# Kernel optimization log

Hardware: AMD Instinct MI355X
Metric: run time of the kernel (lower is better)

## Reference

```python
import jax, jax.numpy as jnp
import numpy as np
from jax import lax

N, D, NUM_SPEC, NUM_HOPS = 8192, 256, 32, 3
ETA, EPS, LN_EPS = 0.5, 0.5, 1e-5


def setup_inputs() -> dict:
    key = jax.random.key(0)
    ks = jax.random.split(key, 4)
    H = jax.random.normal(ks[0], (N, D), dtype=jnp.float32)
    # normalized adjacency proxy: scale so spectral norm is O(1) and hops stay stable
    A = jax.random.normal(ks[1], (N, N), dtype=jnp.float32) / jnp.sqrt(jnp.float32(N))
    # orthonormal-ish eigenvector columns
    V = jax.random.normal(ks[2], (N, NUM_SPEC), dtype=jnp.float32)
    V = V / jnp.linalg.norm(V, axis=0, keepdims=True)
    eigvals = jax.random.uniform(ks[3], (NUM_SPEC,), dtype=jnp.float32, maxval=2.0)
    return {
        "H": H,
        "A": A,
        "V": V,
        "eigvals": eigvals,
        "spec_logits": jnp.zeros((NUM_SPEC,), jnp.float32),
        "lap_logits": jnp.full((NUM_SPEC,), 0.1, jnp.float32),
        "hop_weights": jnp.full((NUM_HOPS + 1,), 1.0 / (NUM_HOPS + 1), jnp.float32),
        "threshold": jnp.full((D,), 0.05, jnp.float32),
        "ln_gamma": jnp.ones((D,), jnp.float32),
        "ln_beta": jnp.zeros((D,), jnp.float32),
    }


def reference(H, A, V, eigvals, spec_logits, lap_logits, hop_weights, threshold, ln_gamma, ln_beta):
    n, d = H.shape
    num_hops = hop_weights.shape[0] - 1

    # hop propagation: hops[k] = A^k H, shape [K, n, d] with K = num_hops+1
    def step(Hc, _):
        Hn = A @ Hc
        return Hn, Hn
    _, rest = lax.scan(step, H, None, length=num_hops)
    hops = jnp.concatenate([H[None], rest], axis=0)  # [K, n, d]

    hop_w = jax.nn.softmax(hop_weights)          # [K]
    spec_w = jax.nn.softmax(spec_logits)         # [S]
    lap_lams = jax.nn.softplus(lap_logits)       # [S]
    coeff = jnp.float32(d) / (jnp.float32(n) * jnp.float32(EPS) ** 2)

    # Phi[k,s,:] = v_s^T H_k  -> batched rank-1 projections
    Phi = jnp.einsum('ns,knd->ksd', V, hops)     # [K, S, d]

    # M = I + coeff * phi phi^T, batched small [d,d] SPD solves
    eye = jnp.eye(d, dtype=H.dtype)
    M = eye + coeff * jnp.einsum('ksi,ksj->ksij', Phi, Phi)  # [K,S,d,d]
    # phi @ M^{-1} == M^{-1} phi (M symmetric)
    q = coeff * jnp.linalg.solve(M, Phi[..., None])[..., 0]  # [K,S,d]

    # grad_R_total = sum_{k,s} hop_w[k] spec_w[s] v_s q_{k,s}^T = V @ T_R
    T_R = spec_w[:, None] * jnp.einsum('k,ksd->sd', hop_w, q)       # [S,d]
    grad_R = V @ T_R                                                 # [n,d]

    # grad_L_total = sum_{k,s} hop_w[k] lap_lams[s] eig_s v_s phi_{k,s}^T
    T_L = (lap_lams * eigvals)[:, None] * jnp.einsum('k,ksd->sd', hop_w, Phi)
    grad_L = V @ T_L

    H_half = H + ETA * grad_R - ETA * grad_L

    # soft threshold (proximal L1)
    thr = threshold[None, :]
    H_out = jnp.sign(H_half) * jax.nn.relu(jnp.abs(H_half) - thr)

    # LayerNorm over last dim
    mu = jnp.mean(H_out, axis=-1, keepdims=True)
    var = jnp.var(H_out, axis=-1, keepdims=True)
    H_out = (H_out - mu) / jnp.sqrt(var + LN_EPS) * ln_gamma + ln_beta
    return (H_out, lax.stop_gradient(hop_w), lax.stop_gradient(spec_w))
```

## Files before the change

kernel.cpp:

```cpp
#include <hip/hip_runtime.h>
#include <hip/hip_bf16.h>
#include <stdint.h>

#define NN 8192
#define DIM 256
#define NSPEC 32
#define ETA 0.5f
#define COEFF 0.125f
#define LNEPS 1e-5f

typedef __attribute__((ext_vector_type(8))) short bf16x8;
typedef __attribute__((ext_vector_type(4))) float f32x4;

__device__ __forceinline__ unsigned short bf2u(__hip_bfloat16 b) {
    union { __hip_bfloat16 b; unsigned short u; } c; c.b = b; return c.u;
}
__device__ __forceinline__ __hip_bfloat16 u2bf(unsigned short u) {
    union { __hip_bfloat16 b; unsigned short u; } c; c.u = u; return c.b;
}

__device__ __forceinline__ void async16(const void* g, void* l) {
    __builtin_amdgcn_global_load_lds(
        (const __attribute__((address_space(1))) void*)g,
        (__attribute__((address_space(3))) void*)l, 16, 0, 0);
}

__global__ void castT_A(const float* __restrict__ A, __hip_bfloat16* __restrict__ AT) {
    __shared__ unsigned short tile[64 * 66];
    int r0 = blockIdx.x * 64, c0 = blockIdx.y * 64;
    int t = threadIdx.x;
    for (int i = 0; i < 16; ++i) {
        int idx = i * 256 + t;
        int r = idx >> 6, c = idx & 63;
        tile[r * 66 + c] = bf2u(__float2bfloat16(A[(long)(r0 + r) * NN + c0 + c]));
    }
    __syncthreads();
    for (int i = 0; i < 16; ++i) {
        int idx = i * 256 + t;
        int c = idx >> 6, r = idx & 63;
        AT[(long)(c0 + c) * NN + r0 + r] = u2bf(tile[r * 66 + c]);
    }
}

__global__ void trans_V(const float* __restrict__ V, __hip_bfloat16* __restrict__ VT) {
    __shared__ float tile[64 * 33];
    int n0 = blockIdx.x * 64;
    int t = threadIdx.x;
    for (int i = 0; i < 8; ++i) {
        int idx = i * 256 + t;
        tile[(idx >> 5) * 33 + (idx & 31)] = V[(long)(n0 + (idx >> 5)) * NSPEC + (idx & 31)];
    }
    __syncthreads();
    for (int i = 0; i < 8; ++i) {
        int idx = i * 256 + t;
        int s = idx >> 6, r = idx & 63;
        VT[(long)s * NN + n0 + r] = __float2bfloat16(tile[r * 33 + s]);
    }
}

#define BM 128
#define BKH 128
#define HSPLIT 8
#define HKC (NN / HSPLIT)
#define HITERS (HKC / BKH)

__launch_bounds__(256, 2)
__global__ void gemm_hopW(const __hip_bfloat16* __restrict__ AT,
                          const __hip_bfloat16* __restrict__ WT,
                          float* __restrict__ P) {
    __shared__ __align__(16) __hip_bfloat16 As[2][BM * BKH];
    __shared__ __align__(16) __hip_bfloat16 Ws[2][NSPEC * BKH];
    const int t = threadIdx.x;
    const int w = t >> 6, l = t & 63;
    const int wm = w & 1, wn = w >> 1;
    const long gm0 = (long)blockIdx.x * BM;
    const long kbase = (long)blockIdx.y * HKC;

    const int lr4 = l >> 4;
    const int lg = l & 15;

    auto stage = [&](int buf, long kpos) {
#pragma unroll
        for (int c = 0; c < 8; ++c) {
            int rb = w * 32 + c * 4;
            int row = rb + lr4;
            async16(AT + (gm0 + row) * (long)NN + kpos + ((lg ^ (row & 15)) << 3),
                    &As[buf][rb * BKH]);
        }
#pragma unroll
        for (int c = 0; c < 2; ++c) {
            int rb = w * 8 + c * 4;
            int row = rb + lr4;
            async16(WT + (long)row * NN + kpos + ((lg ^ (row & 15)) << 3),
                    &Ws[buf][rb * BKH]);
        }
    };

    f32x4 acc[4];
#pragma unroll
    for (int mt = 0; mt < 4; ++mt) acc[mt] = (f32x4){0.f, 0.f, 0.f, 0.f};

    const int rowq = l & 15;
    const int kq = l >> 4;

    stage(0, kbase);
    for (int kt = 0; kt < HITERS; ++kt) {
        __syncthreads();
        const int cur = kt & 1;
        if (kt + 1 < HITERS) stage(cur ^ 1, kbase + (long)(kt + 1) * BKH);

#pragma unroll
        for (int ks = 0; ks < 4; ++ks) {
            const int pg = ((ks * 4 + kq) ^ rowq) << 3;
            bf16x8 bfrag = *(const bf16x8*)&Ws[cur][(wn * 16 + rowq) * BKH + pg];
#pragma unroll
            for (int mt = 0; mt < 4; ++mt) {
                bf16x8 afrag = *(const bf16x8*)&As[cur][(wm * 64 + mt * 16 + rowq) * BKH + pg];
                acc[mt] = __builtin_amdgcn_mfma_f32_16x16x32_bf16(afrag, bfrag, acc[mt], 0, 0, 0);
            }
        }
    }

    float* Pz = P + (long)blockIdx.y * NN * NSPEC;
    const int s = wn * 16 + (l & 15);
#pragma unroll
    for (int mt = 0; mt < 4; ++mt)
#pragma unroll
        for (int r = 0; r < 4; ++r) {
            long m = gm0 + wm * 64 + mt * 16 + (l >> 4) * 4 + r;
            Pz[m * NSPEC + s] = acc[mt][r];
        }
}

__global__ void reduce_W(const float* __restrict__ P, float* __restrict__ Wf,
                         __hip_bfloat16* __restrict__ WTbf) {
    __shared__ float tile[64 * 33];
    int n0 = blockIdx.x * 64;
    int t = threadIdx.x;
    for (int i = 0; i < 8; ++i) {
        int idx = i * 256 + t;
        int r = idx >> 5, s = idx & 31;
        long off = (long)(n0 + r) * NSPEC + s;
        float v = 0.f;
#pragma unroll
        for (int z = 0; z < HSPLIT; ++z) v += P[(long)z * NN * NSPEC + off];
        Wf[off] = v;
        tile[r * 33 + s] = v;
    }
    __syncthreads();
    for (int i = 0; i < 8; ++i) {
        int idx = i * 256 + t;
        int s = idx >> 6, r = idx & 63;
        WTbf[(long)s * NN + n0 + r] = __float2bfloat16(tile[r * 33 + s]);
    }
}

__global__ void phi_kernel(const float* __restrict__ W0, const float* __restrict__ W1,
                           const float* __restrict__ W2, const float* __restrict__ W3,
                           const float* __restrict__ H, float* __restrict__ Phi) {
    __shared__ float ldsW[64 * NSPEC];
    int t = threadIdx.x;
    int s0 = (t >> 6) * 8;
    int d0 = (t & 63) * 4;
    int n0 = blockIdx.x * 128;
    int k = blockIdx.y;
    const float* W = (k == 0) ? W0 : (k == 1) ? W1 : (k == 2) ? W2 : W3;
    float4 acc[8];
#pragma unroll
    for (int j = 0; j < 8; ++j) acc[j] = (float4){0.f, 0.f, 0.f, 0.f};

    for (int tile = 0; tile < 2; ++tile) {
        int nb = n0 + tile * 64;
#pragma unroll
        for (int i = 0; i < 8; ++i) {
            int idx = i * 256 + t;
            ldsW[idx] = W[(long)(nb + (idx >> 5)) * NSPEC + (idx & 31)];
        }
        __syncthreads();
        for (int nn = 0; nn < 64; ++nn) {
            float4 x = *(const float4*)&H[(long)(nb + nn) * DIM + d0];
#pragma unroll
            for (int j = 0; j < 8; ++j) {
                float vs = ldsW[nn * NSPEC + s0 + j];
                acc[j].x += vs * x.x; acc[j].y += vs * x.y;
                acc[j].z += vs * x.z; acc[j].w += vs * x.w;
            }
        }
        __syncthreads();
    }
#pragma unroll
    for (int j = 0; j < 8; ++j) {
        float* ph = &Phi[((k * NSPEC) + s0 + j) * DIM + d0];
        atomicAdd(ph + 0, acc[j].x);
        atomicAdd(ph + 1, acc[j].y);
        atomicAdd(ph + 2, acc[j].z);
        atomicAdd(ph + 3, acc[j].w);
    }
}

__global__ void tc_kernel(const float* __restrict__ Phi,
                          const float* __restrict__ eigvals,
                          const float* __restrict__ spec_logits,
                          const float* __restrict__ lap_logits,
                          const float* __restrict__ hop_weights,
                          float* __restrict__ Tc,
                          float* __restrict__ out_tail) {
    int s = blockIdx.x, t = threadIdx.x;
    float hw0 = hop_weights[0], hw1 = hop_weights[1], hw2 = hop_weights[2], hw3 = hop_weights[3];
    float hm = fmaxf(fmaxf(hw0, hw1), fmaxf(hw2, hw3));
    hw0 = expf(hw0 - hm); hw1 = expf(hw1 - hm); hw2 = expf(hw2 - hm); hw3 = expf(hw3 - hm);
    float hs = hw0 + hw1 + hw2 + hw3;
    hw0 /= hs; hw1 /= hs; hw2 /= hs; hw3 /= hs;
    float hw[4] = {hw0, hw1, hw2, hw3};
    float sm = -1e30f;
    for (int j = 0; j < NSPEC; ++j) sm = fmaxf(sm, spec_logits[j]);
    float ssum = 0.f;
    for (int j = 0; j < NSPEC; ++j) ssum += expf(spec_logits[j] - sm);
    float spec_w_s = expf(spec_logits[s] - sm) / ssum;
    float lp = lap_logits[s];
    float lap = (lp > 20.f) ? lp : log1pf(expf(lp));
    float le = lap * eigvals[s];

    __shared__ float red[4];
    float accR = 0.f, accL = 0.f;
    for (int k = 0; k < 4; ++k) {
        float phi = Phi[(k * NSPEC + s) * DIM + t];
        float v = phi * phi;
        for (int off = 32; off; off >>= 1) v += __shfl_xor(v, off);
        if ((t & 63) == 0) red[t >> 6] = v;
        __syncthreads();
        float ssq = red[0] + red[1] + red[2] + red[3];
        __syncthreads();
        float q = COEFF * phi / (1.f + COEFF * ssq);
        accR += hw[k] * q;
        accL += hw[k] * phi;
    }
    Tc[s * DIM + t] = spec_w_s * accR - le * accL;
    if (s == 0) {
        if (t < 4) out_tail[t] = hw[t];
        if (t < NSPEC) out_tail[4 + t] = expf(spec_logits[t] - sm) / ssum;
    }
}

__launch_bounds__(256)
__global__ void final_kernel(const float* __restrict__ H, const float* __restrict__ V,
                             const float* __restrict__ Tc, const float* __restrict__ thr,
                             const float* __restrict__ gamma, const float* __restrict__ beta,
                             float* __restrict__ out) {
    __shared__ float tc[NSPEC * DIM];
    int t = threadIdx.x;
    {
        const float4* s4 = (const float4*)Tc;
        float4* d4 = (float4*)tc;
        for (int i = 0; i < 8; ++i) d4[i * 256 + t] = s4[i * 256 + t];
    }
    __syncthreads();
    int w = t >> 6, l = t & 63;
    long row = (long)blockIdx.x * 4 + w;
    int d0 = l * 4;
    const float* vrow = V + row * NSPEC;
    float4 G = {0.f, 0.f, 0.f, 0.f};
#pragma unroll 8
    for (int s = 0; s < NSPEC; ++s) {
        float vs = vrow[s];
        float4 c4 = *(const float4*)&tc[s * DIM + d0];
        G.x += vs * c4.x; G.y += vs * c4.y; G.z += vs * c4.z; G.w += vs * c4.w;
    }
    float4 h = *(const float4*)&H[row * DIM + d0];
    float4 th = *(const float4*)&thr[d0];
    float y[4];
    y[0] = h.x + ETA * G.x; y[1] = h.y + ETA * G.y;
    y[2] = h.z + ETA * G.z; y[3] = h.w + ETA * G.w;
    float tv[4] = {th.x, th.y, th.z, th.w};
    float s1 = 0.f, s2 = 0.f;
#pragma unroll
    for (int j = 0; j < 4; ++j) {
        float a = fabsf(y[j]) - tv[j];
        y[j] = (a > 0.f) ? copysignf(a, y[j]) : 0.f;
        s1 += y[j];
        s2 += y[j] * y[j];
    }
    for (int off = 32; off; off >>= 1) { s1 += __shfl_xor(s1, off); s2 += __shfl_xor(s2, off); }
    float mean = s1 * (1.f / DIM);
    float var = s2 * (1.f / DIM) - mean * mean;
    float inv = rsqrtf(var + LNEPS);
    float4 g4 = *(const float4*)&gamma[d0];
    float4 b4 = *(const float4*)&beta[d0];
    float4 o;
    o.x = (y[0] - mean) * inv * g4.x + b4.x;
    o.y = (y[1] - mean) * inv * g4.y + b4.y;
    o.z = (y[2] - mean) * inv * g4.z + b4.z;
    o.w = (y[3] - mean) * inv * g4.w + b4.w;
    *(float4*)&out[row * DIM + d0] = o;
}

extern "C" void kernel_launch(void* const* d_in, const int* in_sizes, int n_in,
                              void* d_out, int out_size, void* d_ws, size_t ws_size,
                              hipStream_t stream) {
    const float* H = (const float*)d_in[0];
    const float* A = (const float*)d_in[1];
    const float* V = (const float*)d_in[2];
    const float* eigvals = (const float*)d_in[3];
    const float* spec_logits = (const float*)d_in[4];
    const float* lap_logits = (const float*)d_in[5];
    const float* hop_weights = (const float*)d_in[6];
    const float* threshold = (const float*)d_in[7];
    const float* ln_gamma = (const float*)d_in[8];
    const float* ln_beta = (const float*)d_in[9];

    char* ws = (char*)d_ws;
    __hip_bfloat16* ATbf = (__hip_bfloat16*)ws;
    float*          P    = (float*)(ws + 134217728);
    __hip_bfloat16* VTbf = (__hip_bfloat16*)(ws + 142606336);
    float* W1f = (float*)(ws + 143130624);
    float* W2f = (float*)(ws + 144179200);
    float* W3f = (float*)(ws + 145227776);
    __hip_bfloat16* W1T = (__hip_bfloat16*)(ws + 146276352);
    __hip_bfloat16* W2T = (__hip_bfloat16*)(ws + 146800640);
    __hip_bfloat16* W3T = (__hip_bfloat16*)(ws + 147324928);
    float* Phi = (float*)(ws + 147849216);
    float* Tc  = (float*)(ws + 147980288);
    float* out = (float*)d_out;

    hipMemsetAsync(Phi, 0, 4 * NSPEC * DIM * sizeof(float), stream);
    castT_A<<<dim3(128, 128), 256, 0, stream>>>(A, ATbf);
    trans_V<<<128, 256, 0, stream>>>(V, VTbf);

    gemm_hopW<<<dim3(64, HSPLIT), 256, 0, stream>>>(ATbf, VTbf, P);
    reduce_W<<<128, 256, 0, stream>>>(P, W1f, W1T);
    gemm_hopW<<<dim3(64, HSPLIT), 256, 0, stream>>>(ATbf, W1T, P);
    reduce_W<<<128, 256, 0, stream>>>(P, W2f, W2T);
    gemm_hopW<<<dim3(64, HSPLIT), 256, 0, stream>>>(ATbf, W2T, P);
    reduce_W<<<128, 256, 0, stream>>>(P, W3f, W3T);

    phi_kernel<<<dim3(64, 4), 256, 0, stream>>>(V, W1f, W2f, W3f, H, Phi);
    tc_kernel<<<NSPEC, 256, 0, stream>>>(Phi, eigvals, spec_logits, lap_logits, hop_weights,
                                         Tc, out + (long)NN * DIM);
    final_kernel<<<2048, 256, 0, stream>>>(H, V, Tc, threshold, ln_gamma, ln_beta, out);
}
```

Measured before the change: 607.1 us.

## Replace bf16 transposed-A MFMA GEMMs with direct fp32 A^T W streaming kernel

Drops the up-front cast-and-transpose of the 8192x8192 A matrix to bf16 and the bf16 MFMA GEMM. A new fp32 FMA kernel instead reads A directly in its original layout, computing A^T W through coalesced row reads with W staged in LDS, split across 32 K-chunks. A simple reduction then sums the partials. This removes a full pass that read and rewrote A and restores fp32 precision, but each hop now streams 256 MB of fp32 A instead of 128 MB of bf16, and uses scalar FMAs rather than matrix cores.

```diff
diff --git a/kernel.cpp b/kernel.cpp
--- a/kernel.cpp
+++ b/kernel.cpp
@@ -1,158 +1,72 @@
 #include <hip/hip_runtime.h>
-#include <hip/hip_bf16.h>
 #include <stdint.h>
 
 #define NN 8192
 #define DIM 256
 #define NSPEC 32
+#define ZSPLIT 32
+#define MCH (NN / ZSPLIT)
 #define ETA 0.5f
 #define COEFF 0.125f
 #define LNEPS 1e-5f
 
-typedef __attribute__((ext_vector_type(8))) short bf16x8;
-typedef __attribute__((ext_vector_type(4))) float f32x4;
-
-__device__ __forceinline__ unsigned short bf2u(__hip_bfloat16 b) {
-    union { __hip_bfloat16 b; unsigned short u; } c; c.b = b; return c.u;
-}
-__device__ __forceinline__ __hip_bfloat16 u2bf(unsigned short u) {
-    union { __hip_bfloat16 b; unsigned short u; } c; c.u = u; return c.b;
-}
-
-__device__ __forceinline__ void async16(const void* g, void* l) {
-    __builtin_amdgcn_global_load_lds(
-        (const __attribute__((address_space(1))) void*)g,
-        (__attribute__((address_space(3))) void*)l, 16, 0, 0);
-}
-
-__global__ void castT_A(const float* __restrict__ A, __hip_bfloat16* __restrict__ AT) {
-    __shared__ unsigned short tile[64 * 66];
-    int r0 = blockIdx.x * 64, c0 = blockIdx.y * 64;
-    int t = threadIdx.x;
-    for (int i = 0; i < 16; ++i) {
-        int idx = i * 256 + t;
-        int r = idx >> 6, c = idx & 63;
-        tile[r * 66 + c] = bf2u(__float2bfloat16(A[(long)(r0 + r) * NN + c0 + c]));
-    }
-    __syncthreads();
-    for (int i = 0; i < 16; ++i) {
-        int idx = i * 256 + t;
-        int c = idx >> 6, r = idx & 63;
-        AT[(long)(c0 + c) * NN + r0 + r] = u2bf(tile[r * 66 + c]);
-    }
-}
-
-__global__ void trans_V(const float* __restrict__ V, __hip_bfloat16* __restrict__ VT) {
-    __shared__ float tile[64 * 33];
-    int n0 = blockIdx.x * 64;
-    int t = threadIdx.x;
+__launch_bounds__(256, 4)
+__global__ void gemm_ATW(const float* __restrict__ A, const float* __restrict__ W,
+                         float* __restrict__ P) {
+    __shared__ float ldsW[MCH * NSPEC];
+    const int t = threadIdx.x;
+    const int w = t >> 6, l = t & 63;
+    const long n0 = (long)blockIdx.x * 256;
+    const int  m0 = blockIdx.y * MCH;
+
+#pragma unroll
     for (int i = 0; i < 8; ++i) {
         int idx = i * 256 + t;
-        tile[(idx >> 5) * 33 + (idx & 31)] = V[(long)(n0 + (idx >> 5)) * NSPEC + (idx & 31)];
+        *(float4*)&ldsW[idx * 4] = *(const float4*)&W[(long)m0 * NSPEC + idx * 4];
     }
     __syncthreads();
-    for (int i = 0; i < 8; ++i) {
-        int idx = i * 256 + t;
-        int s = idx >> 6, r = idx & 63;
-        VT[(long)s * NN + n0 + r] = __float2bfloat16(tile[r * 33 + s]);
-    }
-}
-
-#define BM 128
-#define BKH 128
-#define HSPLIT 8
-#define HKC (NN / HSPLIT)
-#define HITERS (HKC / BKH)
-
-__launch_bounds__(256, 2)
-__global__ void gemm_hopW(const __hip_bfloat16* __restrict__ AT,
-                          const __hip_bfloat16* __restrict__ WT,
-                          float* __restrict__ P) {
-    __shared__ __align__(16) __hip_bfloat16 As[2][BM * BKH];
-    __shared__ __align__(16) __hip_bfloat16 Ws[2][NSPEC * BKH];
-    const int t = threadIdx.x;
-    const int w = t >> 6, l = t & 63;
-    const int wm = w & 1, wn = w >> 1;
-    const long gm0 = (long)blockIdx.x * BM;
-    const long kbase = (long)blockIdx.y * HKC;
-
-    const int lr4 = l >> 4;
-    const int lg = l & 15;
-
-    auto stage = [&](int buf, long kpos) {
-#pragma unroll
-        for (int c = 0; c < 8; ++c) {
-            int rb = w * 32 + c * 4;
-            int row = rb + lr4;
-            async16(AT + (gm0 + row) * (long)NN + kpos + ((lg ^ (row & 15)) << 3),
-                    &As[buf][rb * BKH]);
-        }
-#pragma unroll
-        for (int c = 0; c < 2; ++c) {
-            int rb = w * 8 + c * 4;
-            int row = rb + lr4;
-            async16(WT + (long)row * NN + kpos + ((lg ^ (row & 15)) << 3),
-                    &Ws[buf][rb * BKH]);
-        }
-    };
-
-    f32x4 acc[4];
-#pragma unroll
-    for (int mt = 0; mt < 4; ++mt) acc[mt] = (f32x4){0.f, 0.f, 0.f, 0.f};
-
-    const int rowq = l & 15;
-    const int kq = l >> 4;
-
-    stage(0, kbase);
-    for (int kt = 0; kt < HITERS; ++kt) {
-        __syncthreads();
-        const int cur = kt & 1;
-        if (kt + 1 < HITERS) stage(cur ^ 1, kbase + (long)(kt + 1) * BKH);
-
-#pragma unroll
-        for (int ks = 0; ks < 4; ++ks) {
-            const int pg = ((ks * 4 + kq) ^ rowq) << 3;
-            bf16x8 bfrag = *(const bf16x8*)&Ws[cur][(wn * 16 + rowq) * BKH + pg];
-#pragma unroll
-            for (int mt = 0; mt < 4; ++mt) {
-                bf16x8 afrag = *(const bf16x8*)&As[cur][(wm * 64 + mt * 16 + rowq) * BKH + pg];
-                acc[mt] = __builtin_amdgcn_mfma_f32_16x16x32_bf16(afrag, bfrag, acc[mt], 0, 0, 0);
-            }
-        }
-    }
-
-    float* Pz = P + (long)blockIdx.y * NN * NSPEC;
-    const int s = wn * 16 + (l & 15);
-#pragma unroll
-    for (int mt = 0; mt < 4; ++mt)
-#pragma unroll
-        for (int r = 0; r < 4; ++r) {
-            long m = gm0 + wm * 64 + mt * 16 + (l >> 4) * 4 + r;
-            Pz[m * NSPEC + s] = acc[mt][r];
-        }
-}
-
-__global__ void reduce_W(const float* __restrict__ P, float* __restrict__ Wf,
-                         __hip_bfloat16* __restrict__ WTbf) {
-    __shared__ float tile[64 * 33];
-    int n0 = blockIdx.x * 64;
+
+    float acc[4][8];
+#pragma unroll
+    for (int j = 0; j < 4; ++j)
+#pragma unroll
+        for (int k = 0; k < 8; ++k) acc[j][k] = 0.f;
+
+    const float* Arow = A + (long)m0 * NN + n0 + l * 4;
+    const float* wrow = ldsW + w * 8;
+#pragma unroll 4
+    for (int im = 0; im < MCH; ++im) {
+        float4 a4 = *(const float4*)(Arow + (long)im * NN);
+        float4 w0 = *(const float4*)(wrow + im * NSPEC);
+        float4 w1 = *(const float4*)(wrow + im * NSPEC + 4);
+        float a[4]  = {a4.x, a4.y, a4.z, a4.w};
+        float ww[8] = {w0.x, w0.y, w0.z, w0.w, w1.x, w1.y, w1.z, w1.w};
+#pragma unroll
+        for (int j = 0; j < 4; ++j)
+#pragma unroll
+            for (int k = 0; k < 8; ++k)
+                acc[j][k] += a[j] * ww[k];
+    }
+
+    float* Pp = P + ((n0 + l * 4) * ZSPLIT + blockIdx.y) * NSPEC + w * 8;
+#pragma unroll
+    for (int j = 0; j < 4; ++j) {
+        float4 o0 = {acc[j][0], acc[j][1], acc[j][2], acc[j][3]};
+        float4 o1 = {acc[j][4], acc[j][5], acc[j][6], acc[j][7]};
+        *(float4*)&Pp[(long)j * ZSPLIT * NSPEC] = o0;
+        *(float4*)&Pp[(long)j * ZSPLIT * NSPEC + 4] = o1;
+    }
+}
+
+__global__ void reduce32(const float* __restrict__ P, float* __restrict__ Wf) {
     int t = threadIdx.x;
-    for (int i = 0; i < 8; ++i) {
-        int idx = i * 256 + t;
-        int r = idx >> 5, s = idx & 31;
-        long off = (long)(n0 + r) * NSPEC + s;
-        float v = 0.f;
-#pragma unroll
-        for (int z = 0; z < HSPLIT; ++z) v += P[(long)z * NN * NSPEC + off];
-        Wf[off] = v;
-        tile[r * 33 + s] = v;
-    }
-    __syncthreads();
-    for (int i = 0; i < 8; ++i) {
-        int idx = i * 256 + t;
-        int s = idx >> 6, r = idx & 63;
-        WTbf[(long)s * NN + n0 + r] = __float2bfloat16(tile[r * 33 + s]);
-    }
+    long n = (long)blockIdx.x * 8 + (t >> 5);
+    int s = t & 31;
+    const float* p = P + n * (ZSPLIT * NSPEC) + s;
+    float v = 0.f;
+#pragma unroll
+    for (int z = 0; z < ZSPLIT; ++z) v += p[z * NSPEC];
+    Wf[n * NSPEC + s] = v;
 }
 
 __global__ void phi_kernel(const float* __restrict__ W0, const float* __restrict__ W1,
@@ -309,29 +223,22 @@
     const float* ln_beta = (const float*)d_in[9];
 
     char* ws = (char*)d_ws;
-    __hip_bfloat16* ATbf = (__hip_bfloat16*)ws;
-    float*          P    = (float*)(ws + 134217728);
-    __hip_bfloat16* VTbf = (__hip_bfloat16*)(ws + 142606336);
-    float* W1f = (float*)(ws + 143130624);
-    float* W2f = (float*)(ws + 144179200);
-    float* W3f = (float*)(ws + 145227776);
-    __hip_bfloat16* W1T = (__hip_bfloat16*)(ws + 146276352);
-    __hip_bfloat16* W2T = (__hip_bfloat16*)(ws + 146800640);
-    __hip_bfloat16* W3T = (__hip_bfloat16*)(ws + 147324928);
-    float* Phi = (float*)(ws + 147849216);
-    float* Tc  = (float*)(ws + 147980288);
+    float* P   = (float*)ws;
+    float* W1f = (float*)(ws + 33554432);
+    float* W2f = (float*)(ws + 34603008);
+    float* W3f = (float*)(ws + 35651584);
+    float* Phi = (float*)(ws + 36700160);
+    float* Tc  = (float*)(ws + 36831232);
     float* out = (float*)d_out;
 
     hipMemsetAsync(Phi, 0, 4 * NSPEC * DIM * sizeof(float), stream);
-    castT_A<<<dim3(128, 128), 256, 0, stream>>>(A, ATbf);
-    trans_V<<<128, 256, 0, stream>>>(V, VTbf);
-
-    gemm_hopW<<<dim3(64, HSPLIT), 256, 0, stream>>>(ATbf, VTbf, P);
-    reduce_W<<<128, 256, 0, stream>>>(P, W1f, W1T);
-    gemm_hopW<<<dim3(64, HSPLIT), 256, 0, stream>>>(ATbf, W1T, P);
-    reduce_W<<<128, 256, 0, stream>>>(P, W2f, W2T);
-    gemm_hopW<<<dim3(64, HSPLIT), 256, 0, stream>>>(ATbf, W2T, P);
-    reduce_W<<<128, 256, 0, stream>>>(P, W3f, W3T);
+
+    gemm_ATW<<<dim3(32, ZSPLIT), 256, 0, stream>>>(A, V, P);
+    reduce32<<<1024, 256, 0, stream>>>(P, W1f);
+    gemm_ATW<<<dim3(32, ZSPLIT), 256, 0, stream>>>(A, W1f, P);
+    reduce32<<<1024, 256, 0, stream>>>(P, W2f);
+    gemm_ATW<<<dim3(32, ZSPLIT), 256, 0, stream>>>(A, W2f, P);
+    reduce32<<<1024, 256, 0, stream>>>(P, W3f);
 
     phi_kernel<<<dim3(64, 4), 256, 0, stream>>>(V, W1f, W2f, W3f, H, Phi);
     tc_kernel<<<NSPEC, 256, 0, stream>>>(Phi, eigvals, spec_logits, lap_logits, hop_weights,
```

Result: slower. 643.2 us (+5.9%).
